# Kernel optimization log

Measured on AMD Instinct MI355X. Metric: run time of the kernel, lower is better.

Reference implementation:

```python
import jax, jax.numpy as jnp
import numpy as np
from jax import lax

EPS = 1e-6


def setup_inputs() -> dict:
    key = jax.random.key(0)
    k1, = jax.random.split(key, 1)
    B, T, F = 32, 4096, 256
    inputs = jax.random.uniform(k1, (B, T, F), dtype=jnp.float32)
    # learned scalar params (shape [1]) per PCEN.__init__ initializers
    gain = jnp.array([0.98], dtype=jnp.float32)
    bias = jnp.array([2.0], dtype=jnp.float32)
    root = jnp.array([2.0], dtype=jnp.float32)
    smooth = jnp.array([0.04], dtype=jnp.float32)  # EMA 'smooth' weight
    return {"inputs": inputs, "gain": gain, "bias": bias, "root": root, "smooth": smooth}


def _ema(inputs, smooth):
    # inputs: [B, T, F]; EMA over time with initial_state = inputs[:, 0, :]
    w = jnp.clip(smooth, 0.0, 1.0)  # [1]
    xs = jnp.transpose(inputs, (1, 0, 2))  # [T, B, F]

    def step(a, x):
        a = w * x + (1.0 - w) * a
        return a, a

    _, ys = lax.scan(step, inputs[:, 0, :], xs)  # ys: [T, B, F]
    return jnp.transpose(ys, (1, 0, 2))  # [B, T, F]


def reference(inputs, gain, bias, root, smooth):
    g = jnp.minimum(gain, 1.0)
    r = jnp.maximum(root, 1.0)
    ema = _ema(inputs, smooth)
    one_over_root = 1.0 / r
    out = (inputs / (EPS + ema) ** g + bias) ** one_over_root - bias ** one_over_root
    # normalize_minmax: global min/max over the whole tensor
    mx = jnp.max(out)
    mn = jnp.min(out)
    return 2.0 * ((out - mn) / (mx - mn)) - 1.0
```

## Files before the change

kernel.cpp:

```cpp
#include <hip/hip_runtime.h>

constexpr int B_ = 32;
constexpr int T_ = 4096;
constexpr int F_ = 256;
constexpr int CHUNKS = 64;
constexpr int L_ = T_ / CHUNKS;
constexpr float EPS_ = 1e-6f;

__device__ __forceinline__ unsigned f2ord(float f) {
    unsigned u = __float_as_uint(f);
    return (u & 0x80000000u) ? ~u : (u | 0x80000000u);
}
__device__ __forceinline__ float ord2f(unsigned u) {
    return (u & 0x80000000u) ? __uint_as_float(u ^ 0x80000000u)
                             : __uint_as_float(~u);
}

__device__ __forceinline__ float clamp01(float v) {
    return fminf(fmaxf(v, 0.0f), 1.0f);
}

__global__ __launch_bounds__(64) void ema_chunk_local(
        const float* __restrict__ x, const float* __restrict__ smooth,
        float* __restrict__ E) {
    const int bc = blockIdx.x;
    const int lane = threadIdx.x;
    const float w = clamp01(smooth[0]);
    const float d = 1.0f - w;

    const float4* xp = reinterpret_cast<const float4*>(
                           x + (size_t)bc * L_ * F_) + lane;
    float4 a = make_float4(0.f, 0.f, 0.f, 0.f);

    for (int t0 = 0; t0 < L_; t0 += 8) {
        float4 v[8];
#pragma unroll
        for (int i = 0; i < 8; ++i) v[i] = xp[(size_t)(t0 + i) * (F_ / 4)];
#pragma unroll
        for (int i = 0; i < 8; ++i) {
            a.x = fmaf(w, v[i].x, d * a.x);
            a.y = fmaf(w, v[i].y, d * a.y);
            a.z = fmaf(w, v[i].z, d * a.z);
            a.w = fmaf(w, v[i].w, d * a.w);
        }
    }
    reinterpret_cast<float4*>(E + (size_t)bc * F_)[lane] = a;
}

__global__ __launch_bounds__(64) void ema_carry(
        const float* __restrict__ x, const float* __restrict__ smooth,
        const float* __restrict__ E, float* __restrict__ In,
        unsigned* __restrict__ mm) {
    const int b = blockIdx.x;
    const int lane = threadIdx.x;
    if (b == 0 && lane == 0) {
        mm[0] = 0xFFFFFFFFu;
        mm[1] = 0x00000000u;
    }
    const float w = clamp01(smooth[0]);
    const float d = 1.0f - w;
    float dL = d;
    dL *= dL;
    dL *= dL;
    dL *= dL;
    dL *= dL;
    dL *= dL;
    dL *= dL;

    float4 cur = reinterpret_cast<const float4*>(
                     x + (size_t)b * T_ * F_)[lane];
    for (int c = 0; c < CHUNKS; ++c) {
        const size_t idx = ((size_t)b * CHUNKS + c) * (F_ / 4) + lane;
        reinterpret_cast<float4*>(In)[idx] = cur;
        const float4 e = reinterpret_cast<const float4*>(E)[idx];
        cur.x = fmaf(dL, cur.x, e.x);
        cur.y = fmaf(dL, cur.y, e.y);
        cur.z = fmaf(dL, cur.z, e.z);
        cur.w = fmaf(dL, cur.w, e.w);
    }
}

__device__ __forceinline__ float pcen_elem(float xv, float av, float g,
                                           float inv_r, float bias,
                                           float bpow) {
    const float p = __builtin_exp2f(-g * __builtin_log2f(EPS_ + av));
    const float base = fmaf(xv, p, bias);
    return __builtin_exp2f(inv_r * __builtin_log2f(base)) - bpow;
}

__global__ __launch_bounds__(64) void pcen_out(
        const float* __restrict__ x, const float* __restrict__ In,
        const float* __restrict__ gain, const float* __restrict__ bias_p,
        const float* __restrict__ root, const float* __restrict__ smooth,
        float* __restrict__ out, unsigned* __restrict__ mm) {
    const int bc = blockIdx.x;
    const int lane = threadIdx.x;
    const float w = clamp01(smooth[0]);
    const float d = 1.0f - w;
    const float g = fminf(gain[0], 1.0f);
    const float r = fmaxf(root[0], 1.0f);
    const float inv_r = 1.0f / r;
    const float bias = bias_p[0];
    const float bpow = __builtin_exp2f(inv_r * __builtin_log2f(bias));

    const float4* xp = reinterpret_cast<const float4*>(
                           x + (size_t)bc * L_ * F_) + lane;
    float4* op = reinterpret_cast<float4*>(
                     out + (size_t)bc * L_ * F_) + lane;
    float4 a = reinterpret_cast<const float4*>(In)[(size_t)bc * (F_ / 4) + lane];

    float lmin = __builtin_inff(), lmax = -__builtin_inff();
    for (int t0 = 0; t0 < L_; t0 += 8) {
        float4 v[8];
#pragma unroll
        for (int i = 0; i < 8; ++i) v[i] = xp[(size_t)(t0 + i) * (F_ / 4)];
#pragma unroll
        for (int i = 0; i < 8; ++i) {
            a.x = fmaf(w, v[i].x, d * a.x);
            a.y = fmaf(w, v[i].y, d * a.y);
            a.z = fmaf(w, v[i].z, d * a.z);
            a.w = fmaf(w, v[i].w, d * a.w);
            float4 o;
            o.x = pcen_elem(v[i].x, a.x, g, inv_r, bias, bpow);
            o.y = pcen_elem(v[i].y, a.y, g, inv_r, bias, bpow);
            o.z = pcen_elem(v[i].z, a.z, g, inv_r, bias, bpow);
            o.w = pcen_elem(v[i].w, a.w, g, inv_r, bias, bpow);
            lmin = fminf(lmin, fminf(fminf(o.x, o.y), fminf(o.z, o.w)));
            lmax = fmaxf(lmax, fmaxf(fmaxf(o.x, o.y), fmaxf(o.z, o.w)));
            op[(size_t)(t0 + i) * (F_ / 4)] = o;
        }
    }
#pragma unroll
    for (int off = 32; off > 0; off >>= 1) {
        lmin = fminf(lmin, __shfl_xor(lmin, off));
        lmax = fmaxf(lmax, __shfl_xor(lmax, off));
    }
    if (lane == 0) {
        atomicMin(&mm[0], f2ord(lmin));
        atomicMax(&mm[1], f2ord(lmax));
    }
}

__global__ __launch_bounds__(256) void norm_apply(
        float* __restrict__ out, const unsigned* __restrict__ mm, int n4) {
    const float mn = ord2f(mm[0]);
    const float mx = ord2f(mm[1]);
    const float s = 2.0f / (mx - mn);
    const float o = fmaf(-mn, s, -1.0f);
    float4* p = reinterpret_cast<float4*>(out);
    const int stride = gridDim.x * blockDim.x;
    for (int i = blockIdx.x * blockDim.x + threadIdx.x; i < n4; i += stride) {
        float4 v = p[i];
        v.x = fmaf(v.x, s, o);
        v.y = fmaf(v.y, s, o);
        v.z = fmaf(v.z, s, o);
        v.w = fmaf(v.w, s, o);
        p[i] = v;
    }
}

extern "C" void kernel_launch(void* const* d_in, const int* in_sizes, int n_in,
                              void* d_out, int out_size, void* d_ws, size_t ws_size,
                              hipStream_t stream) {
    const float* x      = (const float*)d_in[0];
    const float* gain   = (const float*)d_in[1];
    const float* bias   = (const float*)d_in[2];
    const float* root   = (const float*)d_in[3];
    const float* smooth = (const float*)d_in[4];
    float* out = (float*)d_out;

    float* E  = (float*)d_ws;
    float* In = E + (size_t)B_ * CHUNKS * F_;
    unsigned* mm = (unsigned*)(In + (size_t)B_ * CHUNKS * F_);

    ema_chunk_local<<<B_ * CHUNKS, 64, 0, stream>>>(x, smooth, E);
    ema_carry<<<B_, 64, 0, stream>>>(x, smooth, E, In, mm);
    pcen_out<<<B_ * CHUNKS, 64, 0, stream>>>(x, In, gain, bias, root, smooth,
                                             out, mm);
    norm_apply<<<2048, 256, 0, stream>>>(out, mm, (B_ * T_ * F_) / 4);
}
```

Before: 337.9 us.

## Fuse PCEN pipeline into one cooperative kernel and recompute output instead of normalizing

Replaces the four separate launches (chunk-local EMA, carry, PCEN output, normalize) with a single cooperative kernel that uses grid-wide syncs between phases. The final phase recomputes the EMA and PCEN values from the input and applies the min/max normalization directly. This removes the write of unnormalized output and its later read-modify-write pass. The costs are a third read of the input, transcendentals evaluated twice, three grid barriers, and a serial carry phase where only 32 waves do work while the rest wait.

```diff
diff --git a/kernel.cpp b/kernel.cpp
--- a/kernel.cpp
+++ b/kernel.cpp
@@ -1,4 +1,7 @@
 #include <hip/hip_runtime.h>
+#include <hip/hip_cooperative_groups.h>
+
+namespace cg = cooperative_groups;
 
 constexpr int B_ = 32;
 constexpr int T_ = 4096;
@@ -6,6 +9,8 @@
 constexpr int CHUNKS = 64;
 constexpr int L_ = T_ / CHUNKS;
 constexpr float EPS_ = 1e-6f;
+constexpr int WAVES_PER_BLOCK = 4;
+constexpr int NBLOCKS = (B_ * CHUNKS) / WAVES_PER_BLOCK;
 
 __device__ __forceinline__ unsigned f2ord(float f) {
     unsigned u = __float_as_uint(f);
@@ -15,69 +20,8 @@
     return (u & 0x80000000u) ? __uint_as_float(u ^ 0x80000000u)
                              : __uint_as_float(~u);
 }
-
 __device__ __forceinline__ float clamp01(float v) {
     return fminf(fmaxf(v, 0.0f), 1.0f);
-}
-
-__global__ __launch_bounds__(64) void ema_chunk_local(
-        const float* __restrict__ x, const float* __restrict__ smooth,
-        float* __restrict__ E) {
-    const int bc = blockIdx.x;
-    const int lane = threadIdx.x;
-    const float w = clamp01(smooth[0]);
-    const float d = 1.0f - w;
-
-    const float4* xp = reinterpret_cast<const float4*>(
-                           x + (size_t)bc * L_ * F_) + lane;
-    float4 a = make_float4(0.f, 0.f, 0.f, 0.f);
-
-    for (int t0 = 0; t0 < L_; t0 += 8) {
-        float4 v[8];
-#pragma unroll
-        for (int i = 0; i < 8; ++i) v[i] = xp[(size_t)(t0 + i) * (F_ / 4)];
-#pragma unroll
-        for (int i = 0; i < 8; ++i) {
-            a.x = fmaf(w, v[i].x, d * a.x);
-            a.y = fmaf(w, v[i].y, d * a.y);
-            a.z = fmaf(w, v[i].z, d * a.z);
-            a.w = fmaf(w, v[i].w, d * a.w);
-        }
-    }
-    reinterpret_cast<float4*>(E + (size_t)bc * F_)[lane] = a;
-}
-
-__global__ __launch_bounds__(64) void ema_carry(
-        const float* __restrict__ x, const float* __restrict__ smooth,
-        const float* __restrict__ E, float* __restrict__ In,
-        unsigned* __restrict__ mm) {
-    const int b = blockIdx.x;
-    const int lane = threadIdx.x;
-    if (b == 0 && lane == 0) {
-        mm[0] = 0xFFFFFFFFu;
-        mm[1] = 0x00000000u;
-    }
-    const float w = clamp01(smooth[0]);
-    const float d = 1.0f - w;
-    float dL = d;
-    dL *= dL;
-    dL *= dL;
-    dL *= dL;
-    dL *= dL;
-    dL *= dL;
-    dL *= dL;
-
-    float4 cur = reinterpret_cast<const float4*>(
-                     x + (size_t)b * T_ * F_)[lane];
-    for (int c = 0; c < CHUNKS; ++c) {
-        const size_t idx = ((size_t)b * CHUNKS + c) * (F_ / 4) + lane;
-        reinterpret_cast<float4*>(In)[idx] = cur;
-        const float4 e = reinterpret_cast<const float4*>(E)[idx];
-        cur.x = fmaf(dL, cur.x, e.x);
-        cur.y = fmaf(dL, cur.y, e.y);
-        cur.z = fmaf(dL, cur.z, e.z);
-        cur.w = fmaf(dL, cur.w, e.w);
-    }
 }
 
 __device__ __forceinline__ float pcen_elem(float xv, float av, float g,
@@ -88,13 +32,25 @@
     return __builtin_exp2f(inv_r * __builtin_log2f(base)) - bpow;
 }
 
-__global__ __launch_bounds__(64) void pcen_out(
-        const float* __restrict__ x, const float* __restrict__ In,
-        const float* __restrict__ gain, const float* __restrict__ bias_p,
-        const float* __restrict__ root, const float* __restrict__ smooth,
-        float* __restrict__ out, unsigned* __restrict__ mm) {
-    const int bc = blockIdx.x;
-    const int lane = threadIdx.x;
+__device__ __forceinline__ void ema_step(float4& a, const float4& v, float w,
+                                         float d) {
+    a.x = fmaf(w, v.x, d * a.x);
+    a.y = fmaf(w, v.y, d * a.y);
+    a.z = fmaf(w, v.z, d * a.z);
+    a.w = fmaf(w, v.w, d * a.w);
+}
+
+__global__ __launch_bounds__(256) void pcen_fused(
+        const float* __restrict__ x, const float* __restrict__ gain,
+        const float* __restrict__ bias_p, const float* __restrict__ root,
+        const float* __restrict__ smooth, float* __restrict__ out,
+        float* __restrict__ E, float* __restrict__ In,
+        unsigned* __restrict__ mm) {
+    cg::grid_group grid = cg::this_grid();
+    const int wave = threadIdx.x >> 6;
+    const int lane = threadIdx.x & 63;
+    const int bc = blockIdx.x * WAVES_PER_BLOCK + wave;
+
     const float w = clamp01(smooth[0]);
     const float d = 1.0f - w;
     const float g = fminf(gain[0], 1.0f);
@@ -103,59 +59,101 @@
     const float bias = bias_p[0];
     const float bpow = __builtin_exp2f(inv_r * __builtin_log2f(bias));
 
+    if (blockIdx.x == 0 && threadIdx.x == 0) {
+        mm[0] = 0xFFFFFFFFu;
+        mm[1] = 0x00000000u;
+    }
+
     const float4* xp = reinterpret_cast<const float4*>(
                            x + (size_t)bc * L_ * F_) + lane;
-    float4* op = reinterpret_cast<float4*>(
-                     out + (size_t)bc * L_ * F_) + lane;
-    float4 a = reinterpret_cast<const float4*>(In)[(size_t)bc * (F_ / 4) + lane];
+    const size_t fidx = (size_t)bc * (F_ / 4) + lane;
 
-    float lmin = __builtin_inff(), lmax = -__builtin_inff();
-    for (int t0 = 0; t0 < L_; t0 += 8) {
-        float4 v[8];
+    {
+        float4 a = make_float4(0.f, 0.f, 0.f, 0.f);
+        for (int t0 = 0; t0 < L_; t0 += 8) {
+            float4 v[8];
 #pragma unroll
-        for (int i = 0; i < 8; ++i) v[i] = xp[(size_t)(t0 + i) * (F_ / 4)];
+            for (int i = 0; i < 8; ++i) v[i] = xp[(size_t)(t0 + i) * (F_ / 4)];
 #pragma unroll
-        for (int i = 0; i < 8; ++i) {
-            a.x = fmaf(w, v[i].x, d * a.x);
-            a.y = fmaf(w, v[i].y, d * a.y);
-            a.z = fmaf(w, v[i].z, d * a.z);
-            a.w = fmaf(w, v[i].w, d * a.w);
-            float4 o;
-            o.x = pcen_elem(v[i].x, a.x, g, inv_r, bias, bpow);
-            o.y = pcen_elem(v[i].y, a.y, g, inv_r, bias, bpow);
-            o.z = pcen_elem(v[i].z, a.z, g, inv_r, bias, bpow);
-            o.w = pcen_elem(v[i].w, a.w, g, inv_r, bias, bpow);
-            lmin = fminf(lmin, fminf(fminf(o.x, o.y), fminf(o.z, o.w)));
-            lmax = fmaxf(lmax, fmaxf(fmaxf(o.x, o.y), fmaxf(o.z, o.w)));
-            op[(size_t)(t0 + i) * (F_ / 4)] = o;
+            for (int i = 0; i < 8; ++i) ema_step(a, v[i], w, d);
+        }
+        reinterpret_cast<float4*>(E)[fidx] = a;
+    }
+    grid.sync();
+
+    if (bc < B_) {
+        const int b = bc;
+        float dL = d;
+        dL *= dL; dL *= dL; dL *= dL; dL *= dL; dL *= dL; dL *= dL;
+        float4 cur = reinterpret_cast<const float4*>(
+                         x + (size_t)b * T_ * F_)[lane];
+        for (int c = 0; c < CHUNKS; ++c) {
+            const size_t idx = ((size_t)b * CHUNKS + c) * (F_ / 4) + lane;
+            reinterpret_cast<float4*>(In)[idx] = cur;
+            const float4 e = reinterpret_cast<const float4*>(E)[idx];
+            cur.x = fmaf(dL, cur.x, e.x);
+            cur.y = fmaf(dL, cur.y, e.y);
+            cur.z = fmaf(dL, cur.z, e.z);
+            cur.w = fmaf(dL, cur.w, e.w);
         }
     }
+    grid.sync();
+
+    {
+        float4 a = reinterpret_cast<const float4*>(In)[fidx];
+        float lmin = __builtin_inff(), lmax = -__builtin_inff();
+        for (int t0 = 0; t0 < L_; t0 += 8) {
+            float4 v[8];
 #pragma unroll
-    for (int off = 32; off > 0; off >>= 1) {
-        lmin = fminf(lmin, __shfl_xor(lmin, off));
-        lmax = fmaxf(lmax, __shfl_xor(lmax, off));
+            for (int i = 0; i < 8; ++i) v[i] = xp[(size_t)(t0 + i) * (F_ / 4)];
+#pragma unroll
+            for (int i = 0; i < 8; ++i) {
+                ema_step(a, v[i], w, d);
+                float4 o;
+                o.x = pcen_elem(v[i].x, a.x, g, inv_r, bias, bpow);
+                o.y = pcen_elem(v[i].y, a.y, g, inv_r, bias, bpow);
+                o.z = pcen_elem(v[i].z, a.z, g, inv_r, bias, bpow);
+                o.w = pcen_elem(v[i].w, a.w, g, inv_r, bias, bpow);
+                lmin = fminf(lmin, fminf(fminf(o.x, o.y), fminf(o.z, o.w)));
+                lmax = fmaxf(lmax, fmaxf(fmaxf(o.x, o.y), fmaxf(o.z, o.w)));
+            }
+        }
+#pragma unroll
+        for (int off = 32; off > 0; off >>= 1) {
+            lmin = fminf(lmin, __shfl_xor(lmin, off));
+            lmax = fmaxf(lmax, __shfl_xor(lmax, off));
+        }
+        if (lane == 0) {
+            atomicMin(&mm[0], f2ord(lmin));
+            atomicMax(&mm[1], f2ord(lmax));
+        }
     }
-    if (lane == 0) {
-        atomicMin(&mm[0], f2ord(lmin));
-        atomicMax(&mm[1], f2ord(lmax));
-    }
-}
+    __threadfence();
+    grid.sync();
 
-__global__ __launch_bounds__(256) void norm_apply(
-        float* __restrict__ out, const unsigned* __restrict__ mm, int n4) {
-    const float mn = ord2f(mm[0]);
-    const float mx = ord2f(mm[1]);
-    const float s = 2.0f / (mx - mn);
-    const float o = fmaf(-mn, s, -1.0f);
-    float4* p = reinterpret_cast<float4*>(out);
-    const int stride = gridDim.x * blockDim.x;
-    for (int i = blockIdx.x * blockDim.x + threadIdx.x; i < n4; i += stride) {
-        float4 v = p[i];
-        v.x = fmaf(v.x, s, o);
-        v.y = fmaf(v.y, s, o);
-        v.z = fmaf(v.z, s, o);
-        v.w = fmaf(v.w, s, o);
-        p[i] = v;
+    {
+        const float mn = ord2f(((volatile unsigned*)mm)[0]);
+        const float mx = ord2f(((volatile unsigned*)mm)[1]);
+        const float s = 2.0f / (mx - mn);
+        const float off = fmaf(-mn, s, -1.0f);
+        float4* op = reinterpret_cast<float4*>(
+                         out + (size_t)bc * L_ * F_) + lane;
+        float4 a = reinterpret_cast<const float4*>(In)[fidx];
+        for (int t0 = 0; t0 < L_; t0 += 8) {
+            float4 v[8];
+#pragma unroll
+            for (int i = 0; i < 8; ++i) v[i] = xp[(size_t)(t0 + i) * (F_ / 4)];
+#pragma unroll
+            for (int i = 0; i < 8; ++i) {
+                ema_step(a, v[i], w, d);
+                float4 o;
+                o.x = fmaf(pcen_elem(v[i].x, a.x, g, inv_r, bias, bpow), s, off);
+                o.y = fmaf(pcen_elem(v[i].y, a.y, g, inv_r, bias, bpow), s, off);
+                o.z = fmaf(pcen_elem(v[i].z, a.z, g, inv_r, bias, bpow), s, off);
+                o.w = fmaf(pcen_elem(v[i].w, a.w, g, inv_r, bias, bpow), s, off);
+                op[(size_t)(t0 + i) * (F_ / 4)] = o;
+            }
+        }
     }
 }
 
@@ -173,9 +171,9 @@
     float* In = E + (size_t)B_ * CHUNKS * F_;
     unsigned* mm = (unsigned*)(In + (size_t)B_ * CHUNKS * F_);
 
-    ema_chunk_local<<<B_ * CHUNKS, 64, 0, stream>>>(x, smooth, E);
-    ema_carry<<<B_, 64, 0, stream>>>(x, smooth, E, In, mm);
-    pcen_out<<<B_ * CHUNKS, 64, 0, stream>>>(x, In, gain, bias, root, smooth,
-                                             out, mm);
-    norm_apply<<<2048, 256, 0, stream>>>(out, mm, (B_ * T_ * F_) / 4);
+    void* args[] = {(void*)&x, (void*)&gain, (void*)&bias, (void*)&root,
+                    (void*)&smooth, (void*)&out, (void*)&E, (void*)&In,
+                    (void*)&mm};
+    hipLaunchCooperativeKernel((void*)pcen_fused, dim3(NBLOCKS), dim3(256),
+                               args, 0, stream);
 }
```

New measurement: 545.4 us. +61.4%, slower.
